# Performance work log

Measured on AMD Instinct MI355X. Metric: run time of the kernel, lower is better.

## Reference

```python
import jax, jax.numpy as jnp
import numpy as np

B, T, K = 256, 512, 128

def setup_inputs() -> dict:
    key = jax.random.key(0)
    k1, k2, k3, k4, k5 = jax.random.split(key, 5)
    emissions = jax.random.normal(k1, (B, T, K), dtype=jnp.float32)
    tags = jax.random.randint(k2, (B, T), 0, K)
    mask = jnp.ones((B, T), dtype=bool)
    # xavier_uniform_ for trans: limit = sqrt(6/(fan_in+fan_out))
    limit = float(np.sqrt(6.0 / (K + K)))
    trans = jax.random.uniform(k3, (K, K), minval=-limit, maxval=limit, dtype=jnp.float32)
    start = 0.1 * jax.random.normal(k4, (K,), dtype=jnp.float32)
    end = 0.1 * jax.random.normal(k5, (K,), dtype=jnp.float32)
    return {"emissions": emissions, "trans": trans, "start": start, "end": end,
            "tags": tags, "mask": mask}

def reference(emissions, trans, start, end, tags, mask):
    # --- log partition (forward algorithm) via lax.scan over time ---
    em_t = jnp.moveaxis(emissions, 1, 0)  # [T,B,K]
    mk_t = jnp.moveaxis(mask, 1, 0)       # [T,B]
    alpha0 = start + em_t[0]              # [B,K]

    def step(alpha, xs):
        em, mk = xs                                      # em:[B,K], mk:[B]
        scores = alpha[:, :, None] + trans[None] + em[:, None, :]  # [B,K,K]
        alpha_next = jax.nn.logsumexp(scores, axis=1)    # [B,K]
        alpha = jnp.where(mk[:, None], alpha_next, alpha)
        return alpha, None

    alpha, _ = jax.lax.scan(step, alpha0, (em_t[1:], mk_t[1:]))
    logZ = jax.nn.logsumexp(alpha + end, axis=1)  # [B]

    # --- gold path score, fully vectorized ---
    emit = jnp.take_along_axis(emissions, tags[..., None], axis=2)[..., 0]  # [B,T]
    trans_sc = trans[tags[:, :-1], tags[:, 1:]]                             # [B,T-1]
    step_sc = (emit[:, 1:] + trans_sc) * mask[:, 1:]                        # masked steps
    score = start[tags[:, 0]] + emit[:, 0] + jnp.sum(step_sc, axis=1)
    last_idx = jnp.sum(mask, axis=1).astype(jnp.int32) - 1
    last_tags = jnp.take_along_axis(tags, last_idx[:, None], axis=1)[:, 0]
    score = score + end[last_tags]

    return jnp.mean(logZ - score)
```

## Files before the change

kernel.cpp:

```cpp
#include <hip/hip_runtime.h>

#define B_ 256
#define T_ 512
#define K_ 128
#define HALF_T 256

typedef _Float16 half8 __attribute__((ext_vector_type(8)));
typedef _Float16 half2_t __attribute__((ext_vector_type(2)));
typedef float f32x4 __attribute__((ext_vector_type(4)));

__device__ inline float fast_exp2(float x) {
#if __has_builtin(__builtin_amdgcn_exp2f)
    return __builtin_amdgcn_exp2f(x);
#else
    return exp2f(x);
#endif
}
__device__ inline float fast_log2(float x) {
#if __has_builtin(__builtin_amdgcn_logf)
    return __builtin_amdgcn_logf(x);
#else
    return log2f(x);
#endif
}
__device__ inline float dot2(half2_t a, half2_t b, float c) {
#if __has_builtin(__builtin_amdgcn_fdot2)
    return __builtin_amdgcn_fdot2(a, b, c, false);
#else
    return fmaf((float)a.x, (float)b.x, fmaf((float)a.y, (float)b.y, c));
#endif
}
__device__ inline unsigned pack2(float x, float y) {
#if __has_builtin(__builtin_amdgcn_cvt_pkrtz)
    auto h = __builtin_amdgcn_cvt_pkrtz(x, y);
    return __builtin_bit_cast(unsigned, h);
#else
    half2_t h; h.x = (_Float16)x; h.y = (_Float16)y;
    return __builtin_bit_cast(unsigned, h);
#endif
}
__device__ inline half2_t as_h2(unsigned u) {
    return __builtin_bit_cast(half2_t, u);
}

#define WS_TT   0
#define WS_FV   (K_ * K_)
#define WS_BV   (WS_FV + B_ * 64)
#define WS_M2F  (WS_BV + B_ * 64)
#define WS_M2B  (WS_M2F + B_)
#define WS_SCF  (WS_M2B + B_)
#define WS_SCB  (WS_SCF + B_)

__global__ void crf_transpose_kernel(const float* __restrict__ trans,
                                     float* __restrict__ transT)
{
    int idx = blockIdx.x * 256 + threadIdx.x;
    int r = idx >> 7, c = idx & (K_ - 1);
    transT[c * K_ + r] = trans[r * K_ + c];
}


__global__ __launch_bounds__(256, 1)
void crf_half_kernel(const float* __restrict__ emissions,
                     const float* __restrict__ trans,
                     const float* __restrict__ start,
                     const float* __restrict__ endv,
                     const int* __restrict__ tags,
                     unsigned* __restrict__ ws_u32)
{
    const int bid  = blockIdx.x;
    const bool fwd = bid < (B_ / 2);
    const int bp   = fwd ? bid : bid - (B_ / 2);
    const int b0g  = bp * 2;
    const int tid  = threadIdx.x;
    const int wave = tid >> 6;
    const int lane = tid & 63;
    const int l15  = lane & 15;
    const int g4   = lane >> 4;
    const int colbase = (wave << 5) + l15;

    __shared__ __align__(16) _Float16 emlds[2][HALF_T][K_];
    __shared__ __align__(16) _Float16 aebuf[2][2][160];
    __shared__ float wred[4];

    const float* transT = (const float*)(ws_u32 + WS_TT);
    unsigned*    fv     = ws_u32 + WS_FV;
    unsigned*    bv     = ws_u32 + WS_BV;
    float*       m2f    = (float*)(ws_u32 + WS_M2F);
    float*       m2b    = (float*)(ws_u32 + WS_M2B);
    float*       scf    = (float*)(ws_u32 + WS_SCF);
    float*       scb    = (float*)(ws_u32 + WS_SCB);

    const float L  = 1.44269504f;
    const float C2 = 7.7f;

    const float* M   = fwd ? trans : transT;
    const float* sv_ = fwd ? start : endv;
    const int rbase  = fwd ? 0 : HALF_T;
    const int r0     = fwd ? 0 : (HALF_T - 1);
    const int NIT    = fwd ? (HALF_T - 1) : HALF_T;
    const int em_base = fwd ? 0 : (HALF_T - 1);
    const int em_sign = fwd ? 1 : -1;

    {
        const float4* ef4_0 = reinterpret_cast<const float4*>(
            emissions + ((size_t)b0g * T_ + rbase) * K_);
        const float4* ef4_1 = reinterpret_cast<const float4*>(
            emissions + ((size_t)(b0g + 1) * T_ + rbase) * K_);
        #pragma unroll
        for (int rd = 0; rd < 4; ++rd) {
            const float4* src = (rd < 2) ? ef4_0 : ef4_1;
            const int bsel2 = (rd < 2) ? 0 : 1;
            const int base = (rd & 1) * 16;
            float4 tmp[16];
            #pragma unroll
            for (int u = 0; u < 16; ++u)
                tmp[u] = src[(base + u) * 256 + tid];
            #pragma unroll
            for (int u = 0; u < 16; ++u) {
                int f = (base + u) * 256 + tid;
                int r = f >> 5, m = f & 31;
                uint2 w;
                w.x = pack2(tmp[u].x, tmp[u].y);
                w.y = pack2(tmp[u].z, tmp[u].w);
                *reinterpret_cast<uint2*>(&emlds[bsel2][r][4 * m]) = w;
            }
        }
    }

#define EFRAG(kc, nc, dst)                                                  \
    {                                                                       \
        half8 t;                                                            \
        _Pragma("unroll")                                                   \
        for (int i = 0; i < 8; ++i) {                                       \
            int k = (kc) * 32 + g4 * 8 + i;                                 \
            t[i] = (_Float16)fast_exp2(M[k * K_ + colbase + 16 * (nc)] * L);\
        }                                                                   \
        dst = t;                                                            \
    }
    half8 e00, e01, e10, e11, e20, e21, e30, e31;
    EFRAG(0, 0, e00) EFRAG(0, 1, e01)
    EFRAG(1, 0, e10) EFRAG(1, 1, e11)
    EFRAG(2, 0, e20) EFRAG(2, 1, e21)
    EFRAG(3, 0, e30) EFRAG(3, 1, e31)
#undef EFRAG

    __syncthreads();

    {
        int ib = tid >> 7, ij = tid & 127;
        float z = (sv_[ij] + (float)emlds[ib][r0][ij]) * L;
        float mx = z;
        #pragma unroll
        for (int d = 1; d < 64; d <<= 1) mx = fmaxf(mx, __shfl_xor(mx, d));
        if (lane == 0) wred[wave] = mx;
    }
    __syncthreads();
    float M2_0 = fmaxf(wred[0], wred[1]);
    float M2_1 = fmaxf(wred[2], wred[3]);
    {
        int ib = tid >> 7, ij = tid & 127;
        float Mz = ib == 0 ? M2_0 : M2_1;
        float z = (sv_[ij] + (float)emlds[ib][r0][ij]) * L;
        aebuf[0][ib][ij] = (_Float16)fast_exp2(z - Mz);
    }
    __syncthreads();

    const int bsel = lane & 1;
    for (int n = 1; n <= NIT; ++n) {
        const _Float16* aerow = &aebuf[(n - 1) & 1][0][0];

        const char* abase = (const char*)aerow + bsel * 320 + (g4 << 4);
        half8 a0 = *reinterpret_cast<const half8*>(abase);
        half8 a1 = *reinterpret_cast<const half8*>(abase + 64);
        half8 a2 = *reinterpret_cast<const half8*>(abase + 128);
        half8 a3 = *reinterpret_cast<const half8*>(abase + 192);

        uint2 p0 = *reinterpret_cast<const uint2*>(aerow);
        uint2 p1 = *reinterpret_cast<const uint2*>(aerow + 160);

        const int emrow = em_base + em_sign * n;
        float em00 = 0.f, em01 = 0.f, em10 = 0.f, em11 = 0.f;
        if (emrow >= 0) {
            em00 = (float)emlds[0][emrow][colbase];
            em01 = (float)emlds[0][emrow][colbase + 16];
            em10 = (float)emlds[1][emrow][colbase];
            em11 = (float)emlds[1][emrow][colbase + 16];
        }

        f32x4 acc0a = {0.f, 0.f, 0.f, 0.f};
        f32x4 acc0b = {0.f, 0.f, 0.f, 0.f};
        f32x4 acc1a = {0.f, 0.f, 0.f, 0.f};
        f32x4 acc1b = {0.f, 0.f, 0.f, 0.f};
        acc0a = __builtin_amdgcn_mfma_f32_16x16x32_f16(a0, e00, acc0a, 0, 0, 0);
        acc1a = __builtin_amdgcn_mfma_f32_16x16x32_f16(a0, e01, acc1a, 0, 0, 0);
        acc0b = __builtin_amdgcn_mfma_f32_16x16x32_f16(a1, e10, acc0b, 0, 0, 0);
        acc1b = __builtin_amdgcn_mfma_f32_16x16x32_f16(a1, e11, acc1b, 0, 0, 0);
        acc0a = __builtin_amdgcn_mfma_f32_16x16x32_f16(a2, e20, acc0a, 0, 0, 0);
        acc1a = __builtin_amdgcn_mfma_f32_16x16x32_f16(a2, e21, acc1a, 0, 0, 0);
        acc0b = __builtin_amdgcn_mfma_f32_16x16x32_f16(a3, e30, acc0b, 0, 0, 0);
        acc1b = __builtin_amdgcn_mfma_f32_16x16x32_f16(a3, e31, acc1b, 0, 0, 0);

        half2_t q0 = as_h2(p0.x), q1 = as_h2(p0.y);
        float pm0 = fmaxf(fmaxf((float)q0.x, (float)q0.y),
                          fmaxf((float)q1.x, (float)q1.y));
        half2_t r0h = as_h2(p1.x), r1h = as_h2(p1.y);
        float pm1 = fmaxf(fmaxf((float)r0h.x, (float)r0h.y),
                          fmaxf((float)r1h.x, (float)r1h.y));
        pm0 = fmaxf(pm0, 6.1e-5f);
        pm1 = fmaxf(pm1, 6.1e-5f);
        float corr0 = fast_log2(pm0);
        float corr1 = fast_log2(pm1);

        float F00 = fast_exp2(fmaf(em00, L, -C2 - corr0));
        float F01 = fast_exp2(fmaf(em01, L, -C2 - corr0));
        float F10 = fast_exp2(fmaf(em10, L, -C2 - corr1));
        float F11 = fast_exp2(fmaf(em11, L, -C2 - corr1));

        if (g4 == 0) {
            float v00 = acc0a[0] + acc0b[0];
            float v01 = acc1a[0] + acc1b[0];
            float v10 = acc0a[1] + acc0b[1];
            float v11 = acc1a[1] + acc1b[1];
            _Float16* nb = &aebuf[n & 1][0][0];
            nb[colbase]            = (_Float16)(v00 * F00);
            nb[colbase + 16]       = (_Float16)(v01 * F01);
            nb[160 + colbase]      = (_Float16)(v10 * F10);
            nb[160 + colbase + 16] = (_Float16)(v11 * F11);
        }
        M2_0 += C2 + corr0;
        M2_1 += C2 + corr1;
        __syncthreads();
    }

    {
        int ib = tid >> 7, ij = tid & 127;
        _Float16 v = aebuf[NIT & 1][ib][ij];
        unsigned short* dst = (unsigned short*)(fwd ? fv : bv);
        dst[(size_t)(b0g + ib) * 128 + ij] = __builtin_bit_cast(unsigned short, v);
    }
    if (tid == 0) {
        (fwd ? m2f : m2b)[b0g]     = M2_0;
        (fwd ? m2f : m2b)[b0g + 1] = M2_1;
    }

    {
        const int kk = (fwd ? 0 : HALF_T) + tid;
        for (int bi = 0; bi < 2; ++bi) {
            const int*   tg = tags + (size_t)(b0g + bi) * T_;
            const float* eb = emissions + (size_t)(b0g + bi) * T_ * K_;
            int cur = tg[kk];
            float sc = eb[(size_t)kk * K_ + cur];
            if (kk > 0) sc += trans[tg[kk - 1] * K_ + cur];
            if (fwd && kk == 0) sc += start[cur];
            if (!fwd && kk == T_ - 1) sc += endv[cur];
            #pragma unroll
            for (int d = 1; d < 64; d <<= 1) sc += __shfl_xor(sc, d);
            __syncthreads();
            if (lane == 0) wred[wave] = sc;
            __syncthreads();
            if (tid == 0)
                (fwd ? scf : scb)[b0g + bi] =
                    wred[0] + wred[1] + wred[2] + wred[3];
        }
    }
}

__global__ void crf_join_kernel(const unsigned* __restrict__ ws_u32,
                                float* __restrict__ out)
{
    const unsigned* fv  = ws_u32 + WS_FV;
    const unsigned* bv  = ws_u32 + WS_BV;
    const float*    m2f = (const float*)(ws_u32 + WS_M2F);
    const float*    m2b = (const float*)(ws_u32 + WS_M2B);
    const float*    scf = (const float*)(ws_u32 + WS_SCF);
    const float*    scb = (const float*)(ws_u32 + WS_SCB);

    const float LN2 = 0.69314718f;
    int b = threadIdx.x;

    float acc = 0.0f;
    #pragma unroll
    for (int k = 0; k < 64; ++k)
        acc = dot2(as_h2(fv[b * 64 + k]), as_h2(bv[b * 64 + k]), acc);

    float logZ = (m2f[b] + m2b[b] + fast_log2(acc)) * LN2;
    float v = logZ - scf[b] - scb[b];

    #pragma unroll
    for (int d = 1; d < 64; d <<= 1) v += __shfl_xor(v, d);
    __shared__ float w[4];
    if ((threadIdx.x & 63) == 0) w[threadIdx.x >> 6] = v;
    __syncthreads();
    if (threadIdx.x == 0)
        out[0] = (w[0] + w[1] + w[2] + w[3]) * (1.0f / 256.0f);
}

extern "C" void kernel_launch(void* const* d_in, const int* in_sizes, int n_in,
                              void* d_out, int out_size, void* d_ws, size_t ws_size,
                              hipStream_t stream)
{
    const float* emissions = (const float*)d_in[0];
    const float* trans     = (const float*)d_in[1];
    const float* start     = (const float*)d_in[2];
    const float* endv      = (const float*)d_in[3];
    const int*   tags      = (const int*)d_in[4];

    unsigned* ws = (unsigned*)d_ws;

    crf_transpose_kernel<<<K_ * K_ / 256, 256, 0, stream>>>(trans, (float*)(ws + WS_TT));
    crf_half_kernel<<<B_, 256, 0, stream>>>(emissions, trans, start, endv, tags, ws);
    crf_join_kernel<<<1, 256, 0, stream>>>(ws, (float*)d_out);
}
```

Measured before the change: 116.4 us.

## Run CRF recurrence in a single wave to remove per-step block barriers

The serial forward/backward recurrence moves from four waves, which had to meet at a block barrier every time step, into wave 0 alone. That wave holds all 32 exp(trans) MFMA B-fragments in registers and keeps the alpha vector in a single permuted LDS buffer, so only compiler fences are needed between steps. Waves 1-2 load and convert the emissions, wave 3 computes the gold-path score in parallel, and the work done per step by the one wave grows eightfold. It relies on in-wave LDS ordering without a double buffer and puts heavy register pressure on wave 0.

Result: slower. 163.4 us (+40.3%).

```diff
diff --git a/kernel.cpp b/kernel.cpp
--- a/kernel.cpp
+++ b/kernel.cpp
@@ -28,15 +28,6 @@
     return __builtin_amdgcn_fdot2(a, b, c, false);
 #else
     return fmaf((float)a.x, (float)b.x, fmaf((float)a.y, (float)b.y, c));
-#endif
-}
-__device__ inline unsigned pack2(float x, float y) {
-#if __has_builtin(__builtin_amdgcn_cvt_pkrtz)
-    auto h = __builtin_amdgcn_cvt_pkrtz(x, y);
-    return __builtin_bit_cast(unsigned, h);
-#else
-    half2_t h; h.x = (_Float16)x; h.y = (_Float16)y;
-    return __builtin_bit_cast(unsigned, h);
 #endif
 }
 __device__ inline half2_t as_h2(unsigned u) {
@@ -77,11 +68,10 @@
     const int lane = tid & 63;
     const int l15  = lane & 15;
     const int g4   = lane >> 4;
-    const int colbase = (wave << 5) + l15;
+    const int bsel = lane & 1;
 
     __shared__ __align__(16) _Float16 emlds[2][HALF_T][K_];
-    __shared__ __align__(16) _Float16 aebuf[2][2][160];
-    __shared__ float wred[4];
+    __shared__ __align__(16) _Float16 aest[2][K_];
 
     const float* transT = (const float*)(ws_u32 + WS_TT);
     unsigned*    fv     = ws_u32 + WS_FV;
@@ -96,173 +86,184 @@
 
     const float* M   = fwd ? trans : transT;
     const float* sv_ = fwd ? start : endv;
-    const int rbase  = fwd ? 0 : HALF_T;
-    const int r0     = fwd ? 0 : (HALF_T - 1);
-    const int NIT    = fwd ? (HALF_T - 1) : HALF_T;
+    const int rbase   = fwd ? 0 : HALF_T;
+    const int r0      = fwd ? 0 : (HALF_T - 1);
+    const int NIT     = fwd ? (HALF_T - 1) : HALF_T;
     const int em_base = fwd ? 0 : (HALF_T - 1);
     const int em_sign = fwd ? 1 : -1;
 
+    half8 e0_0, e0_1, e0_2, e0_3, e0_4, e0_5, e0_6, e0_7;
+    half8 e1_0, e1_1, e1_2, e1_3, e1_4, e1_5, e1_6, e1_7;
+    half8 e2_0, e2_1, e2_2, e2_3, e2_4, e2_5, e2_6, e2_7;
+    half8 e3_0, e3_1, e3_2, e3_3, e3_4, e3_5, e3_6, e3_7;
+
+    if (wave == 0) {
+#define DEFE(kc, nc)                                                        \
+        {                                                                   \
+            half8 t;                                                        \
+            _Pragma("unroll")                                               \
+            for (int i = 0; i < 8; ++i) {                                   \
+                int pk = (kc) * 32 + g4 * 8 + i;                            \
+                int lk = (pk & 7) * 16 + (pk >> 3);                         \
+                t[i] = (_Float16)fast_exp2(M[lk * K_ + (nc) * 16 + l15] * L); \
+            }                                                               \
+            e##kc##_##nc = t;                                               \
+            asm volatile("" : "+v"(e##kc##_##nc));                          \
+        }
+        DEFE(0,0) DEFE(0,1) DEFE(0,2) DEFE(0,3) DEFE(0,4) DEFE(0,5) DEFE(0,6) DEFE(0,7)
+        DEFE(1,0) DEFE(1,1) DEFE(1,2) DEFE(1,3) DEFE(1,4) DEFE(1,5) DEFE(1,6) DEFE(1,7)
+        DEFE(2,0) DEFE(2,1) DEFE(2,2) DEFE(2,3) DEFE(2,4) DEFE(2,5) DEFE(2,6) DEFE(2,7)
+        DEFE(3,0) DEFE(3,1) DEFE(3,2) DEFE(3,3) DEFE(3,4) DEFE(3,5) DEFE(3,6) DEFE(3,7)
+#undef DEFE
+    } else if (wave < 3) {
+        const int t2 = tid - 64;
+        #pragma unroll
+        for (int rnd = 0; rnd < 16; ++rnd) {
+            float4 tmp[8];
+            #pragma unroll
+            for (int u = 0; u < 8; ++u) {
+                int f = (rnd * 8 + u) * 128 + t2;
+                int bb = f >> 13, rem = f & 8191;
+                const float4* src = reinterpret_cast<const float4*>(
+                    emissions + ((size_t)(b0g + bb) * T_ + rbase) * K_);
+                tmp[u] = src[rem];
+            }
+            #pragma unroll
+            for (int u = 0; u < 8; ++u) {
+                int f = (rnd * 8 + u) * 128 + t2;
+                int bb = f >> 13, rem = f & 8191;
+                int row = rem >> 5, m = rem & 31;
+                #pragma unroll
+                for (int d = 0; d < 4; ++d) {
+                    int j = 4 * m + d;
+                    float v = d == 0 ? tmp[u].x : d == 1 ? tmp[u].y
+                            : d == 2 ? tmp[u].z : tmp[u].w;
+                    emlds[bb][row][(j & 15) * 8 + (j >> 4)] = (_Float16)v;
+                }
+            }
+        }
+    } else {
+        float sc0 = 0.f, sc1 = 0.f;
+        for (int idx = lane; idx < 512; idx += 64) {
+            int bi = idx >> 8;
+            int kk = (idx & 255) + (fwd ? 0 : HALF_T);
+            const int*   tg  = tags + (size_t)(b0g + bi) * T_;
+            const float* eb2 = emissions + (size_t)(b0g + bi) * T_ * K_;
+            int cur = tg[kk];
+            float s = eb2[(size_t)kk * K_ + cur];
+            if (kk > 0) s += trans[tg[kk - 1] * K_ + cur];
+            if (fwd && kk == 0) s += start[cur];
+            if (!fwd && kk == T_ - 1) s += endv[cur];
+            if (bi == 0) sc0 += s; else sc1 += s;
+        }
+        #pragma unroll
+        for (int d = 1; d < 64; d <<= 1) {
+            sc0 += __shfl_xor(sc0, d);
+            sc1 += __shfl_xor(sc1, d);
+        }
+        if (lane == 0) {
+            (fwd ? scf : scb)[b0g]     = sc0;
+            (fwd ? scf : scb)[b0g + 1] = sc1;
+        }
+    }
+
+    __syncthreads();
+
+    if (wave != 0) return;
+
+    float M2_0, M2_1;
     {
-        const float4* ef4_0 = reinterpret_cast<const float4*>(
-            emissions + ((size_t)b0g * T_ + rbase) * K_);
-        const float4* ef4_1 = reinterpret_cast<const float4*>(
-            emissions + ((size_t)(b0g + 1) * T_ + rbase) * K_);
+        int ij0 = lane, ij1 = lane + 64;
+        int p0 = (ij0 & 15) * 8 + (ij0 >> 4);
+        int p1 = (ij1 & 15) * 8 + (ij1 >> 4);
+        float z00 = (sv_[ij0] + (float)emlds[0][r0][p0]) * L;
+        float z01 = (sv_[ij1] + (float)emlds[0][r0][p1]) * L;
+        float z10 = (sv_[ij0] + (float)emlds[1][r0][p0]) * L;
+        float z11 = (sv_[ij1] + (float)emlds[1][r0][p1]) * L;
+        float m0 = fmaxf(z00, z01), m1 = fmaxf(z10, z11);
         #pragma unroll
-        for (int rd = 0; rd < 4; ++rd) {
-            const float4* src = (rd < 2) ? ef4_0 : ef4_1;
-            const int bsel2 = (rd < 2) ? 0 : 1;
-            const int base = (rd & 1) * 16;
-            float4 tmp[16];
-            #pragma unroll
-            for (int u = 0; u < 16; ++u)
-                tmp[u] = src[(base + u) * 256 + tid];
-            #pragma unroll
-            for (int u = 0; u < 16; ++u) {
-                int f = (base + u) * 256 + tid;
-                int r = f >> 5, m = f & 31;
-                uint2 w;
-                w.x = pack2(tmp[u].x, tmp[u].y);
-                w.y = pack2(tmp[u].z, tmp[u].w);
-                *reinterpret_cast<uint2*>(&emlds[bsel2][r][4 * m]) = w;
-            }
-        }
-    }
-
-#define EFRAG(kc, nc, dst)                                                  \
-    {                                                                       \
-        half8 t;                                                            \
-        _Pragma("unroll")                                                   \
-        for (int i = 0; i < 8; ++i) {                                       \
-            int k = (kc) * 32 + g4 * 8 + i;                                 \
-            t[i] = (_Float16)fast_exp2(M[k * K_ + colbase + 16 * (nc)] * L);\
-        }                                                                   \
-        dst = t;                                                            \
-    }
-    half8 e00, e01, e10, e11, e20, e21, e30, e31;
-    EFRAG(0, 0, e00) EFRAG(0, 1, e01)
-    EFRAG(1, 0, e10) EFRAG(1, 1, e11)
-    EFRAG(2, 0, e20) EFRAG(2, 1, e21)
-    EFRAG(3, 0, e30) EFRAG(3, 1, e31)
-#undef EFRAG
-
-    __syncthreads();
-
-    {
-        int ib = tid >> 7, ij = tid & 127;
-        float z = (sv_[ij] + (float)emlds[ib][r0][ij]) * L;
-        float mx = z;
-        #pragma unroll
-        for (int d = 1; d < 64; d <<= 1) mx = fmaxf(mx, __shfl_xor(mx, d));
-        if (lane == 0) wred[wave] = mx;
-    }
-    __syncthreads();
-    float M2_0 = fmaxf(wred[0], wred[1]);
-    float M2_1 = fmaxf(wred[2], wred[3]);
-    {
-        int ib = tid >> 7, ij = tid & 127;
-        float Mz = ib == 0 ? M2_0 : M2_1;
-        float z = (sv_[ij] + (float)emlds[ib][r0][ij]) * L;
-        aebuf[0][ib][ij] = (_Float16)fast_exp2(z - Mz);
-    }
-    __syncthreads();
-
-    const int bsel = lane & 1;
+        for (int d = 1; d < 64; d <<= 1) {
+            m0 = fmaxf(m0, __shfl_xor(m0, d));
+            m1 = fmaxf(m1, __shfl_xor(m1, d));
+        }
+        M2_0 = m0; M2_1 = m1;
+        aest[0][p0] = (_Float16)fast_exp2(z00 - M2_0);
+        aest[0][p1] = (_Float16)fast_exp2(z01 - M2_0);
+        aest[1][p0] = (_Float16)fast_exp2(z10 - M2_1);
+        aest[1][p1] = (_Float16)fast_exp2(z11 - M2_1);
+    }
+
+    const char* abase = (const char*)&aest[0][0] + bsel * 256 + (g4 << 4);
+
     for (int n = 1; n <= NIT; ++n) {
-        const _Float16* aerow = &aebuf[(n - 1) & 1][0][0];
-
-        const char* abase = (const char*)aerow + bsel * 320 + (g4 << 4);
         half8 a0 = *reinterpret_cast<const half8*>(abase);
         half8 a1 = *reinterpret_cast<const half8*>(abase + 64);
         half8 a2 = *reinterpret_cast<const half8*>(abase + 128);
         half8 a3 = *reinterpret_cast<const half8*>(abase + 192);
-
-        uint2 p0 = *reinterpret_cast<const uint2*>(aerow);
-        uint2 p1 = *reinterpret_cast<const uint2*>(aerow + 160);
+        uint2 pr0 = *reinterpret_cast<const uint2*>(&aest[0][0]);
+        uint2 pr1 = *reinterpret_cast<const uint2*>(&aest[1][0]);
 
         const int emrow = em_base + em_sign * n;
-        float em00 = 0.f, em01 = 0.f, em10 = 0.f, em11 = 0.f;
+        half8 em0v = {0,0,0,0,0,0,0,0}, em1v = {0,0,0,0,0,0,0,0};
         if (emrow >= 0) {
-            em00 = (float)emlds[0][emrow][colbase];
-            em01 = (float)emlds[0][emrow][colbase + 16];
-            em10 = (float)emlds[1][emrow][colbase];
-            em11 = (float)emlds[1][emrow][colbase + 16];
-        }
-
-        f32x4 acc0a = {0.f, 0.f, 0.f, 0.f};
-        f32x4 acc0b = {0.f, 0.f, 0.f, 0.f};
-        f32x4 acc1a = {0.f, 0.f, 0.f, 0.f};
-        f32x4 acc1b = {0.f, 0.f, 0.f, 0.f};
-        acc0a = __builtin_amdgcn_mfma_f32_16x16x32_f16(a0, e00, acc0a, 0, 0, 0);
-        acc1a = __builtin_amdgcn_mfma_f32_16x16x32_f16(a0, e01, acc1a, 0, 0, 0);
-        acc0b = __builtin_amdgcn_mfma_f32_16x16x32_f16(a1, e10, acc0b, 0, 0, 0);
-        acc1b = __builtin_amdgcn_mfma_f32_16x16x32_f16(a1, e11, acc1b, 0, 0, 0);
-        acc0a = __builtin_amdgcn_mfma_f32_16x16x32_f16(a2, e20, acc0a, 0, 0, 0);
-        acc1a = __builtin_amdgcn_mfma_f32_16x16x32_f16(a2, e21, acc1a, 0, 0, 0);
-        acc0b = __builtin_amdgcn_mfma_f32_16x16x32_f16(a3, e30, acc0b, 0, 0, 0);
-        acc1b = __builtin_amdgcn_mfma_f32_16x16x32_f16(a3, e31, acc1b, 0, 0, 0);
-
-        half2_t q0 = as_h2(p0.x), q1 = as_h2(p0.y);
+            em0v = *reinterpret_cast<const half8*>(&emlds[0][emrow][l15 * 8]);
+            em1v = *reinterpret_cast<const half8*>(&emlds[1][emrow][l15 * 8]);
+        }
+
+        f32x4 c0 = {0,0,0,0}, c1 = {0,0,0,0}, c2 = {0,0,0,0}, c3 = {0,0,0,0};
+        f32x4 c4 = {0,0,0,0}, c5 = {0,0,0,0}, c6 = {0,0,0,0}, c7 = {0,0,0,0};
+#define MSTEP(kc, A)                                                        \
+        c0 = __builtin_amdgcn_mfma_f32_16x16x32_f16(A, e##kc##_0, c0, 0,0,0); \
+        c1 = __builtin_amdgcn_mfma_f32_16x16x32_f16(A, e##kc##_1, c1, 0,0,0); \
+        c2 = __builtin_amdgcn_mfma_f32_16x16x32_f16(A, e##kc##_2, c2, 0,0,0); \
+        c3 = __builtin_amdgcn_mfma_f32_16x16x32_f16(A, e##kc##_3, c3, 0,0,0); \
+        c4 = __builtin_amdgcn_mfma_f32_16x16x32_f16(A, e##kc##_4, c4, 0,0,0); \
+        c5 = __builtin_amdgcn_mfma_f32_16x16x32_f16(A, e##kc##_5, c5, 0,0,0); \
+        c6 = __builtin_amdgcn_mfma_f32_16x16x32_f16(A, e##kc##_6, c6, 0,0,0); \
+        c7 = __builtin_amdgcn_mfma_f32_16x16x32_f16(A, e##kc##_7, c7, 0,0,0);
+        MSTEP(0, a0) MSTEP(1, a1) MSTEP(2, a2) MSTEP(3, a3)
+#undef MSTEP
+
+        half2_t q0 = as_h2(pr0.x), q1 = as_h2(pr0.y);
         float pm0 = fmaxf(fmaxf((float)q0.x, (float)q0.y),
                           fmaxf((float)q1.x, (float)q1.y));
-        half2_t r0h = as_h2(p1.x), r1h = as_h2(p1.y);
-        float pm1 = fmaxf(fmaxf((float)r0h.x, (float)r0h.y),
-                          fmaxf((float)r1h.x, (float)r1h.y));
+        half2_t s0h = as_h2(pr1.x), s1h = as_h2(pr1.y);
+        float pm1 = fmaxf(fmaxf((float)s0h.x, (float)s0h.y),
+                          fmaxf((float)s1h.x, (float)s1h.y));
         pm0 = fmaxf(pm0, 6.1e-5f);
         pm1 = fmaxf(pm1, 6.1e-5f);
-        float corr0 = fast_log2(pm0);
-        float corr1 = fast_log2(pm1);
-
-        float F00 = fast_exp2(fmaf(em00, L, -C2 - corr0));
-        float F01 = fast_exp2(fmaf(em01, L, -C2 - corr0));
-        float F10 = fast_exp2(fmaf(em10, L, -C2 - corr1));
-        float F11 = fast_exp2(fmaf(em11, L, -C2 - corr1));
-
+        float corr0 = fast_log2(pm0), corr1 = fast_log2(pm1);
+        float k0 = -C2 - corr0, k1 = -C2 - corr1;
+
+        half8 w0, w1;
+#define EPI(nc)                                                             \
+        {                                                                   \
+            float F0 = fast_exp2(fmaf((float)em0v[nc], L, k0));             \
+            float F1 = fast_exp2(fmaf((float)em1v[nc], L, k1));             \
+            w0[nc] = (_Float16)(c##nc[0] * F0);                             \
+            w1[nc] = (_Float16)(c##nc[1] * F1);                             \
+        }
+        EPI(0) EPI(1) EPI(2) EPI(3) EPI(4) EPI(5) EPI(6) EPI(7)
+#undef EPI
         if (g4 == 0) {
-            float v00 = acc0a[0] + acc0b[0];
-            float v01 = acc1a[0] + acc1b[0];
-            float v10 = acc0a[1] + acc0b[1];
-            float v11 = acc1a[1] + acc1b[1];
-            _Float16* nb = &aebuf[n & 1][0][0];
-            nb[colbase]            = (_Float16)(v00 * F00);
-            nb[colbase + 16]       = (_Float16)(v01 * F01);
-            nb[160 + colbase]      = (_Float16)(v10 * F10);
-            nb[160 + colbase + 16] = (_Float16)(v11 * F11);
+            *reinterpret_cast<half8*>(&aest[0][l15 * 8]) = w0;
+            *reinterpret_cast<half8*>(&aest[1][l15 * 8]) = w1;
         }
         M2_0 += C2 + corr0;
         M2_1 += C2 + corr1;
-        __syncthreads();
+        asm volatile("" ::: "memory");
     }
 
     {
-        int ib = tid >> 7, ij = tid & 127;
-        _Float16 v = aebuf[NIT & 1][ib][ij];
-        unsigned short* dst = (unsigned short*)(fwd ? fv : bv);
-        dst[(size_t)(b0g + ib) * 128 + ij] = __builtin_bit_cast(unsigned short, v);
-    }
-    if (tid == 0) {
+        unsigned v0 = *reinterpret_cast<const unsigned*>(&aest[0][lane * 2]);
+        unsigned v1 = *reinterpret_cast<const unsigned*>(&aest[1][lane * 2]);
+        unsigned* dst = fwd ? fv : bv;
+        dst[(size_t)b0g * 64 + lane]       = v0;
+        dst[(size_t)(b0g + 1) * 64 + lane] = v1;
+    }
+    if (lane == 0) {
         (fwd ? m2f : m2b)[b0g]     = M2_0;
         (fwd ? m2f : m2b)[b0g + 1] = M2_1;
-    }
-
-    {
-        const int kk = (fwd ? 0 : HALF_T) + tid;
-        for (int bi = 0; bi < 2; ++bi) {
-            const int*   tg = tags + (size_t)(b0g + bi) * T_;
-            const float* eb = emissions + (size_t)(b0g + bi) * T_ * K_;
-            int cur = tg[kk];
-            float sc = eb[(size_t)kk * K_ + cur];
-            if (kk > 0) sc += trans[tg[kk - 1] * K_ + cur];
-            if (fwd && kk == 0) sc += start[cur];
-            if (!fwd && kk == T_ - 1) sc += endv[cur];
-            #pragma unroll
-            for (int d = 1; d < 64; d <<= 1) sc += __shfl_xor(sc, d);
-            __syncthreads();
-            if (lane == 0) wred[wave] = sc;
-            __syncthreads();
-            if (tid == 0)
-                (fwd ? scf : scb)[b0g + bi] =
-                    wred[0] + wred[1] + wred[2] + wred[3];
-        }
     }
 }
 
```

## Process one sequence per block instead of two, doubling grid size

Applied to the files above, without the earlier changes.

Each block now runs the forward or backward half-recurrence for a single batch element rather than two packed into one MFMA tile, and the grid doubles to 512 blocks. LDS drops to about 64KB per block, so more blocks can be resident per CU and the serial scan latency is spread across more CUs. In exchange, each MFMA now carries only one useful row out of 16, where it used to carry two, so total matrix-core work per sequence doubles.

New measurement: 108.9 us. 6.5% less time.

```diff
diff --git a/kernel.cpp b/kernel.cpp
--- a/kernel.cpp
+++ b/kernel.cpp
@@ -69,9 +69,8 @@
                      unsigned* __restrict__ ws_u32)
 {
     const int bid  = blockIdx.x;
-    const bool fwd = bid < (B_ / 2);
-    const int bp   = fwd ? bid : bid - (B_ / 2);
-    const int b0g  = bp * 2;
+    const bool fwd = bid < B_;
+    const int b    = fwd ? bid : bid - B_;
     const int tid  = threadIdx.x;
     const int wave = tid >> 6;
     const int lane = tid & 63;
@@ -79,8 +78,8 @@
     const int g4   = lane >> 4;
     const int colbase = (wave << 5) + l15;
 
-    __shared__ __align__(16) _Float16 emlds[2][HALF_T][K_];
-    __shared__ __align__(16) _Float16 aebuf[2][2][160];
+    __shared__ __align__(16) _Float16 emlds[HALF_T][K_];
+    __shared__ __align__(16) _Float16 aebuf[2][K_];
     __shared__ float wred[4];
 
     const float* transT = (const float*)(ws_u32 + WS_TT);
@@ -96,34 +95,29 @@
 
     const float* M   = fwd ? trans : transT;
     const float* sv_ = fwd ? start : endv;
-    const int rbase  = fwd ? 0 : HALF_T;
-    const int r0     = fwd ? 0 : (HALF_T - 1);
-    const int NIT    = fwd ? (HALF_T - 1) : HALF_T;
+    const int rbase   = fwd ? 0 : HALF_T;
+    const int r0      = fwd ? 0 : (HALF_T - 1);
+    const int NIT     = fwd ? (HALF_T - 1) : HALF_T;
     const int em_base = fwd ? 0 : (HALF_T - 1);
     const int em_sign = fwd ? 1 : -1;
 
     {
-        const float4* ef4_0 = reinterpret_cast<const float4*>(
-            emissions + ((size_t)b0g * T_ + rbase) * K_);
-        const float4* ef4_1 = reinterpret_cast<const float4*>(
-            emissions + ((size_t)(b0g + 1) * T_ + rbase) * K_);
+        const float4* ef4 = reinterpret_cast<const float4*>(
+            emissions + ((size_t)b * T_ + rbase) * K_);
         #pragma unroll
-        for (int rd = 0; rd < 4; ++rd) {
-            const float4* src = (rd < 2) ? ef4_0 : ef4_1;
-            const int bsel2 = (rd < 2) ? 0 : 1;
-            const int base = (rd & 1) * 16;
+        for (int rd = 0; rd < 2; ++rd) {
             float4 tmp[16];
             #pragma unroll
             for (int u = 0; u < 16; ++u)
-                tmp[u] = src[(base + u) * 256 + tid];
+                tmp[u] = ef4[(rd * 16 + u) * 256 + tid];
             #pragma unroll
             for (int u = 0; u < 16; ++u) {
-                int f = (base + u) * 256 + tid;
+                int f = (rd * 16 + u) * 256 + tid;
                 int r = f >> 5, m = f & 31;
                 uint2 w;
                 w.x = pack2(tmp[u].x, tmp[u].y);
                 w.y = pack2(tmp[u].z, tmp[u].w);
-                *reinterpret_cast<uint2*>(&emlds[bsel2][r][4 * m]) = w;
+                *reinterpret_cast<uint2*>(&emlds[r][4 * m]) = w;
             }
         }
     }
@@ -147,122 +141,89 @@
 
     __syncthreads();
 
+    float M2;
     {
-        int ib = tid >> 7, ij = tid & 127;
-        float z = (sv_[ij] + (float)emlds[ib][r0][ij]) * L;
+        int ij = tid & 127;
+        float z = (sv_[ij] + (float)emlds[r0][ij]) * L;
         float mx = z;
         #pragma unroll
         for (int d = 1; d < 64; d <<= 1) mx = fmaxf(mx, __shfl_xor(mx, d));
         if (lane == 0) wred[wave] = mx;
+        __syncthreads();
+        M2 = fmaxf(fmaxf(wred[0], wred[1]), fmaxf(wred[2], wred[3]));
+        if (tid < K_) aebuf[0][ij] = (_Float16)fast_exp2(z - M2);
     }
     __syncthreads();
-    float M2_0 = fmaxf(wred[0], wred[1]);
-    float M2_1 = fmaxf(wred[2], wred[3]);
-    {
-        int ib = tid >> 7, ij = tid & 127;
-        float Mz = ib == 0 ? M2_0 : M2_1;
-        float z = (sv_[ij] + (float)emlds[ib][r0][ij]) * L;
-        aebuf[0][ib][ij] = (_Float16)fast_exp2(z - Mz);
-    }
-    __syncthreads();
-
-    const int bsel = lane & 1;
+
     for (int n = 1; n <= NIT; ++n) {
-        const _Float16* aerow = &aebuf[(n - 1) & 1][0][0];
-
-        const char* abase = (const char*)aerow + bsel * 320 + (g4 << 4);
+        const _Float16* aerow = aebuf[(n - 1) & 1];
+
+        const char* abase = (const char*)aerow + (g4 << 4);
         half8 a0 = *reinterpret_cast<const half8*>(abase);
         half8 a1 = *reinterpret_cast<const half8*>(abase + 64);
         half8 a2 = *reinterpret_cast<const half8*>(abase + 128);
         half8 a3 = *reinterpret_cast<const half8*>(abase + 192);
 
-        uint2 p0 = *reinterpret_cast<const uint2*>(aerow);
-        uint2 p1 = *reinterpret_cast<const uint2*>(aerow + 160);
+        uint2 pr = *reinterpret_cast<const uint2*>(aerow);
 
         const int emrow = em_base + em_sign * n;
-        float em00 = 0.f, em01 = 0.f, em10 = 0.f, em11 = 0.f;
+        float em0 = 0.f, em1 = 0.f;
         if (emrow >= 0) {
-            em00 = (float)emlds[0][emrow][colbase];
-            em01 = (float)emlds[0][emrow][colbase + 16];
-            em10 = (float)emlds[1][emrow][colbase];
-            em11 = (float)emlds[1][emrow][colbase + 16];
+            em0 = (float)emlds[emrow][colbase];
+            em1 = (float)emlds[emrow][colbase + 16];
         }
 
-        f32x4 acc0a = {0.f, 0.f, 0.f, 0.f};
-        f32x4 acc0b = {0.f, 0.f, 0.f, 0.f};
-        f32x4 acc1a = {0.f, 0.f, 0.f, 0.f};
-        f32x4 acc1b = {0.f, 0.f, 0.f, 0.f};
-        acc0a = __builtin_amdgcn_mfma_f32_16x16x32_f16(a0, e00, acc0a, 0, 0, 0);
-        acc1a = __builtin_amdgcn_mfma_f32_16x16x32_f16(a0, e01, acc1a, 0, 0, 0);
-        acc0b = __builtin_amdgcn_mfma_f32_16x16x32_f16(a1, e10, acc0b, 0, 0, 0);
-        acc1b = __builtin_amdgcn_mfma_f32_16x16x32_f16(a1, e11, acc1b, 0, 0, 0);
-        acc0a = __builtin_amdgcn_mfma_f32_16x16x32_f16(a2, e20, acc0a, 0, 0, 0);
-        acc1a = __builtin_amdgcn_mfma_f32_16x16x32_f16(a2, e21, acc1a, 0, 0, 0);
-        acc0b = __builtin_amdgcn_mfma_f32_16x16x32_f16(a3, e30, acc0b, 0, 0, 0);
-        acc1b = __builtin_amdgcn_mfma_f32_16x16x32_f16(a3, e31, acc1b, 0, 0, 0);
-
-        half2_t q0 = as_h2(p0.x), q1 = as_h2(p0.y);
-        float pm0 = fmaxf(fmaxf((float)q0.x, (float)q0.y),
-                          fmaxf((float)q1.x, (float)q1.y));
-        half2_t r0h = as_h2(p1.x), r1h = as_h2(p1.y);
-        float pm1 = fmaxf(fmaxf((float)r0h.x, (float)r0h.y),
-                          fmaxf((float)r1h.x, (float)r1h.y));
-        pm0 = fmaxf(pm0, 6.1e-5f);
-        pm1 = fmaxf(pm1, 6.1e-5f);
-        float corr0 = fast_log2(pm0);
-        float corr1 = fast_log2(pm1);
-
-        float F00 = fast_exp2(fmaf(em00, L, -C2 - corr0));
-        float F01 = fast_exp2(fmaf(em01, L, -C2 - corr0));
-        float F10 = fast_exp2(fmaf(em10, L, -C2 - corr1));
-        float F11 = fast_exp2(fmaf(em11, L, -C2 - corr1));
+        f32x4 c0a = {0,0,0,0}, c0b = {0,0,0,0};
+        f32x4 c1a = {0,0,0,0}, c1b = {0,0,0,0};
+        c0a = __builtin_amdgcn_mfma_f32_16x16x32_f16(a0, e00, c0a, 0, 0, 0);
+        c1a = __builtin_amdgcn_mfma_f32_16x16x32_f16(a0, e01, c1a, 0, 0, 0);
+        c0b = __builtin_amdgcn_mfma_f32_16x16x32_f16(a1, e10, c0b, 0, 0, 0);
+        c1b = __builtin_amdgcn_mfma_f32_16x16x32_f16(a1, e11, c1b, 0, 0, 0);
+        c0a = __builtin_amdgcn_mfma_f32_16x16x32_f16(a2, e20, c0a, 0, 0, 0);
+        c1a = __builtin_amdgcn_mfma_f32_16x16x32_f16(a2, e21, c1a, 0, 0, 0);
+        c0b = __builtin_amdgcn_mfma_f32_16x16x32_f16(a3, e30, c0b, 0, 0, 0);
+        c1b = __builtin_amdgcn_mfma_f32_16x16x32_f16(a3, e31, c1b, 0, 0, 0);
+
+        half2_t q0 = as_h2(pr.x), q1 = as_h2(pr.y);
+        float pm = fmaxf(fmaxf((float)q0.x, (float)q0.y),
+                         fmaxf((float)q1.x, (float)q1.y));
+        pm = fmaxf(pm, 6.1e-5f);
+        float corr = fast_log2(pm);
+        float F0 = fast_exp2(fmaf(em0, L, -C2 - corr));
+        float F1 = fast_exp2(fmaf(em1, L, -C2 - corr));
 
         if (g4 == 0) {
-            float v00 = acc0a[0] + acc0b[0];
-            float v01 = acc1a[0] + acc1b[0];
-            float v10 = acc0a[1] + acc0b[1];
-            float v11 = acc1a[1] + acc1b[1];
-            _Float16* nb = &aebuf[n & 1][0][0];
-            nb[colbase]            = (_Float16)(v00 * F00);
-            nb[colbase + 16]       = (_Float16)(v01 * F01);
-            nb[160 + colbase]      = (_Float16)(v10 * F10);
-            nb[160 + colbase + 16] = (_Float16)(v11 * F11);
+            _Float16* nb = aebuf[n & 1];
+            nb[colbase]      = (_Float16)((c0a[0] + c0b[0]) * F0);
+            nb[colbase + 16] = (_Float16)((c1a[0] + c1b[0]) * F1);
         }
-        M2_0 += C2 + corr0;
-        M2_1 += C2 + corr1;
-        __syncthreads();
-    }
-
-    {
-        int ib = tid >> 7, ij = tid & 127;
-        _Float16 v = aebuf[NIT & 1][ib][ij];
-        unsigned short* dst = (unsigned short*)(fwd ? fv : bv);
-        dst[(size_t)(b0g + ib) * 128 + ij] = __builtin_bit_cast(unsigned short, v);
-    }
-    if (tid == 0) {
-        (fwd ? m2f : m2b)[b0g]     = M2_0;
-        (fwd ? m2f : m2b)[b0g + 1] = M2_1;
-    }
+        M2 += C2 + corr;
+        __syncthreads();
+    }
+
+    if (tid < 64) {
+        unsigned v = *reinterpret_cast<const unsigned*>(&aebuf[NIT & 1][tid * 2]);
+        (fwd ? fv : bv)[(size_t)b * 64 + tid] = v;
+    }
+    if (tid == 0)
+        (fwd ? m2f : m2b)[b] = M2;
 
     {
         const int kk = (fwd ? 0 : HALF_T) + tid;
-        for (int bi = 0; bi < 2; ++bi) {
-            const int*   tg = tags + (size_t)(b0g + bi) * T_;
-            const float* eb = emissions + (size_t)(b0g + bi) * T_ * K_;
-            int cur = tg[kk];
-            float sc = eb[(size_t)kk * K_ + cur];
-            if (kk > 0) sc += trans[tg[kk - 1] * K_ + cur];
-            if (fwd && kk == 0) sc += start[cur];
-            if (!fwd && kk == T_ - 1) sc += endv[cur];
-            #pragma unroll
-            for (int d = 1; d < 64; d <<= 1) sc += __shfl_xor(sc, d);
-            __syncthreads();
-            if (lane == 0) wred[wave] = sc;
-            __syncthreads();
-            if (tid == 0)
-                (fwd ? scf : scb)[b0g + bi] =
-                    wred[0] + wred[1] + wred[2] + wred[3];
-        }
+        const int*   tg  = tags + (size_t)b * T_;
+        const float* eb2 = emissions + (size_t)b * T_ * K_;
+        int cur = tg[kk];
+        float sc = eb2[(size_t)kk * K_ + cur];
+        if (kk > 0) sc += trans[tg[kk - 1] * K_ + cur];
+        if (fwd && kk == 0) sc += start[cur];
+        if (!fwd && kk == T_ - 1) sc += endv[cur];
+        #pragma unroll
+        for (int d = 1; d < 64; d <<= 1) sc += __shfl_xor(sc, d);
+        __syncthreads();
+        if (lane == 0) wred[wave] = sc;
+        __syncthreads();
+        if (tid == 0)
+            (fwd ? scf : scb)[b] = wred[0] + wred[1] + wred[2] + wred[3];
     }
 }
 
@@ -309,6 +270,6 @@
     unsigned* ws = (unsigned*)d_ws;
 
     crf_transpose_kernel<<<K_ * K_ / 256, 256, 0, stream>>>(trans, (float*)(ws + WS_TT));
-    crf_half_kernel<<<B_, 256, 0, stream>>>(emissions, trans, start, endv, tags, ws);
+    crf_half_kernel<<<2 * B_, 256, 0, stream>>>(emissions, trans, start, endv, tags, ws);
     crf_join_kernel<<<1, 256, 0, stream>>>(ws, (float*)d_out);
 }
```
